# Kernel tuning notes

Hardware: AMD Instinct MI355X
Metric: run time of the kernel (lower is better)

## Reference

```python
import jax, jax.numpy as jnp
import numpy as np

D1 = 4096
D2 = 4096
K = 838860  # int(D1*D2*0.05)
ALPHA = 16.0


def setup_inputs() -> dict:
    key = jax.random.key(0)
    k1, k2, k3, k4, k5 = jax.random.split(key, 5)
    x = jax.random.normal(k1, (2, 64, D1), jnp.float32)
    W_base = jax.random.normal(k2, (D2, D1), jnp.float32) * 0.02  # torch Linear weight (out, in)
    b_base = jnp.zeros((D2,), jnp.float32)
    c_re = jax.random.normal(k3, (K,), jnp.float32) * 0.02
    c_im = jax.random.normal(k4, (K,), jnp.float32) * 0.02
    # unique flat positions of the top-k frequency coefficients (stand-in for topk of |fft2(delta_W_init)|)
    mask_idx = jax.random.permutation(k5, D1 * D2)[:K].astype(jnp.int32)
    return {"x": x, "W_base": W_base, "b_base": b_base,
            "c_re": c_re, "c_im": c_im, "mask_idx": mask_idx}


def reference(x, W_base, b_base, c_re, c_im, mask_idx):
    # scatter sparse complex coefficients into dense frequency matrix
    c = (c_re + 1j * c_im).astype(jnp.complex64)
    F_flat = jnp.zeros((D1 * D2,), jnp.complex64).at[mask_idx].set(c)
    # inverse 2D FFT -> real part -> scale by alpha
    Delta_W = jnp.fft.ifft2(F_flat.reshape(D1, D2)).real.astype(jnp.float32) * ALPHA  # [D1, D2]
    # frozen base linear: h = x @ W_base.T + b
    h = jnp.einsum('bnd,fd->bnf', x, W_base) + b_base
    # LoRA-style low-frequency update
    return h + jnp.einsum('bnd,df->bnf', x, Delta_W)
```

## Files before the change

kernel.cpp:

```cpp
#include <hip/hip_runtime.h>


#define TWO_PI 6.28318530717958647692f
constexpr int NROW = 128;
constexpr float SCALE_A = 16.0f / 16777216.0f;
constexpr int NCHUNK = 256;
constexpr int KC = 8;

typedef unsigned short ushort_t;
using short8 = __attribute__((ext_vector_type(8))) short;
using f32x4  = __attribute__((ext_vector_type(4))) float;

__device__ __forceinline__ ushort_t f2bf(float f) {
  unsigned u = __float_as_uint(f);
  u = (u + 0x7FFFu + ((u >> 16) & 1u)) >> 16;
  return (ushort_t)u;
}

__device__ __forceinline__ unsigned cvtpk(float lo, float hi) {
  unsigned r;
  asm("v_cvt_pk_bf16_f32 %0, %1, %2" : "=v"(r) : "v"(lo), "v"(hi));
  return r;
}

__device__ __forceinline__ void gload_lds16(const void* g, void* l) {
  __builtin_amdgcn_global_load_lds(
      (const __attribute__((address_space(1))) unsigned*)g,
      (__attribute__((address_space(3))) unsigned*)l, 16, 0, 0);
}

__global__ __launch_bounds__(1024) void fused_stage1(const float* __restrict__ x,
                                                     unsigned* __restrict__ XTb,
                                                     const int* __restrict__ idx, int K,
                                                     int chunk, int* __restrict__ cnt) {
  __shared__ __align__(16) char smem[33280];
  const int bx = blockIdx.x, tid = threadIdx.x;
  if (bx < 256) {
    float* xs = (float*)smem;
    float* br = xs + 4096;
    float* bi = br + 2048;
    float2* w64 = (float2*)(bi + 2048);
    const int t = bx & 127, qi = bx >> 7;
    const float* xrow = x + (size_t)t * 4096;
#pragma unroll
    for (int l = 0; l < 4; ++l) xs[tid + 1024 * l] = xrow[tid + 1024 * l];
    if (tid < 64) {
      float s, c; __sincosf(TWO_PI * (float)tid * (1.0f / 64.0f), &s, &c);
      w64[tid] = make_float2(c, s);
    }
    __syncthreads();
#pragma unroll
    for (int l = 0; l < 2; ++l) {
      int o = tid + 1024 * l, m1 = o >> 5, k1l = o & 31, k1 = qi * 32 + k1l;
      float ar = 0.f, ai = 0.f;
      for (int m2 = 0; m2 < 64; ++m2) {
        float xv = xs[m1 + (m2 << 6)];
        float2 w = w64[(m2 * k1) & 63];
        ar = fmaf(xv, w.x, ar); ai = fmaf(xv, w.y, ai);
      }
      float s, c; __sincosf((float)(m1 * k1) * (TWO_PI / 4096.0f), &s, &c);
      br[(m1 << 5) + k1l] = ar * c - ai * s;
      bi[(m1 << 5) + k1l] = ar * s + ai * c;
    }
    __syncthreads();
    {
      const int k1l = tid & 31, k2 = tid >> 5;
      const int k = qi * 32 + k1l + (k2 << 6);
      float xr = 0.f, xi = 0.f;
      for (int m1 = 0; m1 < 64; ++m1) {
        float brv = br[(m1 << 5) + k1l], biv = bi[(m1 << 5) + k1l];
        float2 w = w64[(m1 * k2) & 63];
        xr += brv * w.x - biv * w.y;
        xi += brv * w.y + biv * w.x;
      }
      XTb[(size_t)k * NROW + t] = (unsigned)f2bf(xr) | ((unsigned)f2bf(xi) << 16);
      if (qi == 0 && tid == 0) {
        float xr2 = 0.f, xi2 = 0.f;
        for (int m1 = 0; m1 < 64; ++m1) {
          float sgn = (m1 & 1) ? -1.f : 1.f;
          xr2 = fmaf(sgn, br[m1 << 5], xr2);
          xi2 = fmaf(sgn, bi[m1 << 5], xi2);
        }
        XTb[(size_t)2048 * NROW + t] = (unsigned)f2bf(xr2) | ((unsigned)f2bf(xi2) << 16);
      }
    }
  } else {
    int* h = (int*)smem;
    const int c = bx - 256;
#pragma unroll
    for (int l = 0; l < 4; ++l) h[tid + 1024 * l] = 0;
    __syncthreads();
    const int j0 = c * chunk, j1 = min(j0 + chunk, K);
    for (int j = j0 + tid; j < j1; j += 1024) atomicAdd(&h[idx[j] & 4095], 1);
    __syncthreads();
#pragma unroll
    for (int l = 0; l < 4; ++l) cnt[(size_t)c * 4096 + tid + 1024 * l] = h[tid + 1024 * l];
  }
}

__global__ __launch_bounds__(256) void colscan(int* __restrict__ cnt, int* __restrict__ tot) {
  const int k2 = blockIdx.x * 256 + threadIdx.x;
  int run = 0;
  for (int c8 = 0; c8 < NCHUNK; c8 += 8) {
    int v[8];
#pragma unroll
    for (int i = 0; i < 8; ++i) v[i] = cnt[(size_t)(c8 + i) * 4096 + k2];
#pragma unroll
    for (int i = 0; i < 8; ++i) {
      cnt[(size_t)(c8 + i) * 4096 + k2] = run;
      run += v[i];
    }
  }
  tot[k2] = run;
}

__global__ __launch_bounds__(1024) void scan4096(const int* __restrict__ count,
                                                 int* __restrict__ off) {
  __shared__ int s[4096];
  int tid = threadIdx.x;
#pragma unroll
  for (int l = 0; l < 4; ++l) s[tid + 1024 * l] = count[tid + 1024 * l];
  __syncthreads();
  for (int d = 1; d < 4096; d <<= 1) {
    int v[4];
#pragma unroll
    for (int l = 0; l < 4; ++l) {
      int i = tid + 1024 * l;
      v[l] = s[i] + ((i >= d) ? s[i - d] : 0);
    }
    __syncthreads();
#pragma unroll
    for (int l = 0; l < 4; ++l) s[tid + 1024 * l] = v[l];
    __syncthreads();
  }
#pragma unroll
  for (int l = 0; l < 4; ++l) {
    int i = tid + 1024 * l;
    off[i] = s[i] - count[i];
  }
}

__global__ __launch_bounds__(1024) void scatter2(const int* __restrict__ idx,
                                                 const float* __restrict__ cre,
                                                 const float* __restrict__ cim, int K,
                                                 int chunk, const int* __restrict__ base,
                                                 const int* __restrict__ off,
                                                 uint2* __restrict__ bucket) {
  __shared__ int lbase[4096];
  __shared__ int lcur[4096];
  const int c = blockIdx.x, tid = threadIdx.x;
#pragma unroll
  for (int l = 0; l < 4; ++l) {
    int k2 = tid + 1024 * l;
    lbase[k2] = base[(size_t)c * 4096 + k2] + off[k2];
    lcur[k2] = 0;
  }
  __syncthreads();
  const int j0 = c * chunk, j1 = min(j0 + chunk, K);
  for (int j = j0 + tid; j < j1; j += 1024) {
    int p = idx[j];
    int k2 = p & 4095;
    int r = atomicAdd(&lcur[k2], 1);
    unsigned cr = f2bf(cre[j]), ci = f2bf(cim[j]);
    bucket[lbase[k2] + r] = make_uint2((unsigned)(p >> 12) | (cr << 16), ci << 16);
  }
}

__global__ __launch_bounds__(256, 4) void spmm_col(const uint2* __restrict__ bucket,
                                                   const int* __restrict__ off,
                                                   const int* __restrict__ count,
                                                   const unsigned* __restrict__ XTb,
                                                   float2* __restrict__ Y) {
  __shared__ float4 red[2][64];
  const int lane = threadIdx.x & 63;
  const int wid = threadIdx.x >> 6;
  const int colsel = wid >> 1, half = wid & 1;
  const int k2 = blockIdx.x * 2 + colsel;
  const int s = off[k2], n = count[k2];
  const unsigned voff = lane * 8;
  float ar0 = 0.f, ai0 = 0.f, ar1 = 0.f, ai1 = 0.f;
  for (int c = half * 64; c < n; c += 128) {
    int idx = c + lane;
    uint2 ec = (idx < n) ? bucket[s + idx] : make_uint2(0u, 0u);
#pragma unroll
    for (int g = 0; g < 64; g += 8) {
      unsigned Ap[8], Bp[8];
      uint2 xv0, xv1, xv2, xv3, xv4, xv5, xv6, xv7;
#pragma unroll
      for (int u = 0; u < 8; ++u) {
        unsigned w0 = (unsigned)__builtin_amdgcn_readlane((int)ec.x, g + u);
        unsigned w1 = (unsigned)__builtin_amdgcn_readlane((int)ec.y, g + u);
        int k1 = (int)(w0 & 0xfffu);
        unsigned cj = (k1 > 2048) ? 0x8000u : 0u;
        int r = (k1 > 2048) ? 4096 - k1 : k1;
        unsigned cr16 = w0 >> 16;
        unsigned ci16 = w1 >> 16;
        Ap[u] = cr16 | ((ci16 ^ 0x8000u ^ cj) << 16);
        Bp[u] = ci16 | ((cr16 ^ cj) << 16);
        const unsigned* p = XTb + (size_t)r * NROW;
        uint2* dst = (u == 0) ? &xv0 : (u == 1) ? &xv1 : (u == 2) ? &xv2 :
                     (u == 3) ? &xv3 : (u == 4) ? &xv4 : (u == 5) ? &xv5 :
                     (u == 6) ? &xv6 : &xv7;
        asm volatile("global_load_dwordx2 %0, %1, %2"
                     : "=v"(*dst) : "v"(voff), "s"(p) : "memory");
      }
      asm volatile("s_waitcnt vmcnt(0)"
                   : "+v"(xv0), "+v"(xv1), "+v"(xv2), "+v"(xv3),
                     "+v"(xv4), "+v"(xv5), "+v"(xv6), "+v"(xv7) :: "memory");
      __builtin_amdgcn_sched_barrier(0);
#pragma unroll
      for (int u = 0; u < 8; ++u) {
        uint2 xv = (u == 0) ? xv0 : (u == 1) ? xv1 : (u == 2) ? xv2 :
                   (u == 3) ? xv3 : (u == 4) ? xv4 : (u == 5) ? xv5 :
                   (u == 6) ? xv6 : xv7;
        asm("v_dot2_f32_bf16 %0, %1, %2, %0" : "+v"(ar0) : "v"(Ap[u]), "v"(xv.x));
        asm("v_dot2_f32_bf16 %0, %1, %2, %0" : "+v"(ai0) : "v"(Bp[u]), "v"(xv.x));
        asm("v_dot2_f32_bf16 %0, %1, %2, %0" : "+v"(ar1) : "v"(Ap[u]), "v"(xv.y));
        asm("v_dot2_f32_bf16 %0, %1, %2, %0" : "+v"(ai1) : "v"(Bp[u]), "v"(xv.y));
      }
    }
  }
  if (half == 1) red[colsel][lane] = make_float4(ar0, ai0, ar1, ai1);
  __syncthreads();
  if (half == 0) {
    float4 o = red[colsel][lane];
    ar0 += o.x; ai0 += o.y; ar1 += o.z; ai1 += o.w;
    Y[(size_t)(2 * lane) * 4096 + k2]     = make_float2(ar0, ai0);
    Y[(size_t)(2 * lane + 1) * 4096 + k2] = make_float2(ar1, ai1);
  }
}

__global__ __launch_bounds__(256) void gemm_mfma_partial(const ushort_t* __restrict__ xbf,
                                                         const float* __restrict__ W,
                                                         ushort_t* __restrict__ partb) {
  __shared__ ushort_t xs[128 * 128];
  __shared__ float    wsf[64 * 128];
  const int f0 = blockIdx.x * 64;
  const int kc = blockIdx.y;
  const int tid = threadIdx.x;
  const int w = tid >> 6, lane = tid & 63;

  f32x4 acc[2][4];
#pragma unroll
  for (int i = 0; i < 2; ++i)
#pragma unroll
    for (int j = 0; j < 4; ++j) acc[i][j] = (f32x4){0.f, 0.f, 0.f, 0.f};

  const int kbeg = kc * 512;
  for (int st = 0; st < 4; ++st) {
    const int k0 = kbeg + st * 128;
#pragma unroll
    for (int cc = 0; cc < 8; ++cc) {
      int lb = w * 8192 + cc * 1024;
      int e  = (lb >> 1) + lane * 8;
      int r  = e >> 7;
      int sl = (e >> 3) & 15;
      gload_lds16(xbf + (size_t)r * 4096 + k0 + ((sl ^ (r & 15)) << 3),
                  (char*)xs + lb);
    }
#pragma unroll
    for (int cc = 0; cc < 8; ++cc) {
      int lb = w * 8192 + cc * 1024;
      int e32 = (lb >> 2) + lane * 4;
      int r = e32 >> 7;
      int g = (e32 >> 2) & 31;
      int s8 = g >> 1, h = g & 1;
      gload_lds16(W + (size_t)(f0 + r) * 4096 + k0 + ((s8 ^ (r & 15)) << 3) + (h << 2),
                  (char*)wsf + lb);
    }
    __syncthreads();
#pragma unroll
    for (int kk = 0; kk < 4; ++kk) {
      int ksA = kk * 4 + (lane >> 4);
      short8 af[2], bfr[4];
#pragma unroll
      for (int mf = 0; mf < 2; ++mf) {
        int ra = w * 32 + mf * 16 + (lane & 15);
        af[mf] = *(const short8*)(&xs[ra * 128 + ((ksA ^ (ra & 15)) << 3)]);
      }
#pragma unroll
      for (int nf = 0; nf < 4; ++nf) {
        int rb = nf * 16 + (lane & 15);
        const float* bp = &wsf[rb * 128 + ((ksA ^ (rb & 15)) << 3)];
        float4 a4 = *(const float4*)bp;
        float4 b4 = *(const float4*)(bp + 4);
        union { uint4 u; short8 s; } pk;
        pk.u.x = cvtpk(a4.x, a4.y);
        pk.u.y = cvtpk(a4.z, a4.w);
        pk.u.z = cvtpk(b4.x, b4.y);
        pk.u.w = cvtpk(b4.z, b4.w);
        bfr[nf] = pk.s;
      }
#pragma unroll
      for (int mf = 0; mf < 2; ++mf)
#pragma unroll
        for (int nf = 0; nf < 4; ++nf)
          acc[mf][nf] = __builtin_amdgcn_mfma_f32_16x16x32_bf16(af[mf], bfr[nf], acc[mf][nf], 0, 0, 0);
    }
    __syncthreads();
  }
  ushort_t* pb = partb + ((size_t)kc << 19);
#pragma unroll
  for (int mf = 0; mf < 2; ++mf)
#pragma unroll
    for (int nf = 0; nf < 4; ++nf)
#pragma unroll
      for (int reg = 0; reg < 4; ++reg) {
        int row = w * 32 + mf * 16 + (lane >> 4) * 4 + reg;
        int col = f0 + nf * 16 + (lane & 15);
        pb[(size_t)row * 4096 + col] = f2bf(acc[mf][nf][reg]);
      }
}

__global__ __launch_bounds__(1024) void dft_rows_y(const float2* __restrict__ Y,
                                                   const ushort_t* __restrict__ partb,
                                                   const float* __restrict__ bias,
                                                   float* __restrict__ out) {
  __shared__ float ysr[4096], ysi[4096];
  __shared__ float br[2048], bi[2048];
  __shared__ float2 w64[64];
  const int t = blockIdx.x, qi = blockIdx.y, tid = threadIdx.x;
  const float2* yrow = Y + (size_t)t * 4096;
#pragma unroll
  for (int l = 0; l < 4; ++l) {
    float2 v = yrow[tid + 1024 * l];
    ysr[tid + 1024 * l] = v.x; ysi[tid + 1024 * l] = v.y;
  }
  if (tid < 64) {
    float s, c; __sincosf(TWO_PI * (float)tid * (1.0f / 64.0f), &s, &c);
    w64[tid] = make_float2(c, s);
  }
  __syncthreads();
#pragma unroll
  for (int l = 0; l < 2; ++l) {
    int o = tid + 1024 * l, a = o >> 5, n1l = o & 31, n1 = qi * 32 + n1l;
    float ar = 0.f, ai = 0.f;
    for (int b = 0; b < 64; ++b) {
      float yr = ysr[a + (b << 6)], yi = ysi[a + (b << 6)];
      float2 w = w64[(n1 * b) & 63];
      ar += yr * w.x - yi * w.y;
      ai += yr * w.y + yi * w.x;
    }
    float s, c; __sincosf((float)(n1 * a) * (TWO_PI / 4096.0f), &s, &c);
    br[(a << 5) + n1l] = ar * c - ai * s;
    bi[(a << 5) + n1l] = ar * s + ai * c;
  }
  __syncthreads();
  float* orow = out + (size_t)t * 4096;
  const int n1l = tid & 31;
  const int n1 = qi * 32 + n1l;
#pragma unroll
  for (int l = 0; l < 2; ++l) {
    int n2 = (tid >> 5) + 32 * l;
    float accv = 0.f;
    for (int a = 0; a < 64; ++a) {
      float brv = br[(a << 5) + n1l], biv = bi[(a << 5) + n1l];
      float2 w = w64[(n2 * a) & 63];
      accv += brv * w.x - biv * w.y;
    }
    int o = n1 + (n2 << 6);
    float sum = accv * SCALE_A + bias[o];
#pragma unroll
    for (int i = 0; i < KC; ++i) {
      unsigned uu = partb[((size_t)i << 19) + ((size_t)t << 12) + o];
      sum += __int_as_float((int)(uu << 16));
    }
    orow[o] = sum;
  }
}

__global__ __launch_bounds__(256) void xcvt(const float* __restrict__ x,
                                            ushort_t* __restrict__ xbf) {
  size_t e = ((size_t)blockIdx.x * 256 + threadIdx.x) * 4;
  float4 v = *(const float4*)(x + e);
  unsigned lo = (unsigned)f2bf(v.x) | ((unsigned)f2bf(v.y) << 16);
  unsigned hi = (unsigned)f2bf(v.z) | ((unsigned)f2bf(v.w) << 16);
  *(uint2*)(xbf + e) = make_uint2(lo, hi);
}

extern "C" void kernel_launch(void* const* d_in, const int* in_sizes, int n_in,
                              void* d_out, int out_size, void* d_ws, size_t ws_size,
                              hipStream_t stream) {
  const float* x   = (const float*)d_in[0];
  const float* W   = (const float*)d_in[1];
  const float* b   = (const float*)d_in[2];
  const float* cre = (const float*)d_in[3];
  const float* cim = (const float*)d_in[4];
  const int* midx  = (const int*)d_in[5];
  const int K = in_sizes[3];
  float* out = (float*)d_out;
  const int chunk = (K + NCHUNK - 1) / NCHUNK;

  char* ws = (char*)d_ws;
  unsigned* XTb   = (unsigned*)(ws);
  float2* Y       = (float2*)(ws + ((size_t)2 << 20));
  char* meta      = ws + ((size_t)6 << 20);
  int* tot = (int*)(meta);
  int* off = (int*)(meta + 16384);
  uint2* bucket   = (uint2*)(ws + ((size_t)6 << 20) + 65536);
  int* cnt        = (int*)(ws + ((size_t)13 << 20));
  ushort_t* xbf   = (ushort_t*)(ws + ((size_t)17 << 20));
  ushort_t* partb = (ushort_t*)(ws + ((size_t)6 << 20) + 131072);

  xcvt<<<512, 256, 0, stream>>>(x, xbf);
  fused_stage1<<<512, 1024, 0, stream>>>(x, XTb, midx, K, chunk, cnt);
  colscan<<<16, 256, 0, stream>>>(cnt, tot);
  scan4096<<<1, 1024, 0, stream>>>(tot, off);
  scatter2<<<NCHUNK, 1024, 0, stream>>>(midx, cre, cim, K, chunk, cnt, off, bucket);
  spmm_col<<<2048, 256, 0, stream>>>(bucket, off, tot, XTb, Y);
  gemm_mfma_partial<<<dim3(64, KC), 256, 0, stream>>>(xbf, W, partb);
  dft_rows_y<<<dim3(NROW, 2), 1024, 0, stream>>>(Y, partb, b, out);
}
```

Measured before the change: 125.1 us.

## Fuse spmm with dense GEMM, fold x conversion into stage1, bf16 DFT intermediates

Merges the sparse column SpMM and the split-K MFMA GEMM into one heterogeneous launch so the two independent workloads run concurrently. The GEMM split-K count is halved with smaller K tiles. The x-to-bf16 conversion becomes extra blocks of the stage-1 kernel, removing a launch. DFT intermediates and Y are stored as packed bf16 and reduced with v_dot2_f32_bf16, halving traffic and FMA count at the cost of precision. The partial-sum readback contains a redundant multiply-by-zero term.

```diff
diff --git a/kernel.cpp b/kernel.cpp
--- a/kernel.cpp
+++ b/kernel.cpp
@@ -5,7 +5,7 @@
 constexpr int NROW = 128;
 constexpr float SCALE_A = 16.0f / 16777216.0f;
 constexpr int NCHUNK = 256;
-constexpr int KC = 8;
+constexpr int KC = 4;
 
 typedef unsigned short ushort_t;
 using short8 = __attribute__((ext_vector_type(8))) short;
@@ -16,13 +16,16 @@
   u = (u + 0x7FFFu + ((u >> 16) & 1u)) >> 16;
   return (ushort_t)u;
 }
-
 __device__ __forceinline__ unsigned cvtpk(float lo, float hi) {
   unsigned r;
   asm("v_cvt_pk_bf16_f32 %0, %1, %2" : "=v"(r) : "v"(lo), "v"(hi));
   return r;
 }
-
+__device__ __forceinline__ float bflo(unsigned u) { return __int_as_float((int)(u << 16)); }
+__device__ __forceinline__ float bfhi(unsigned u) { return __int_as_float((int)(u & 0xffff0000u)); }
+__device__ __forceinline__ void dot2(float& acc, unsigned a, unsigned b) {
+  asm("v_dot2_f32_bf16 %0, %1, %2, %0" : "+v"(acc) : "v"(a), "v"(b));
+}
 __device__ __forceinline__ void gload_lds16(const void* g, void* l) {
   __builtin_amdgcn_global_load_lds(
       (const __attribute__((address_space(1))) unsigned*)g,
@@ -32,21 +35,31 @@
 __global__ __launch_bounds__(1024) void fused_stage1(const float* __restrict__ x,
                                                      unsigned* __restrict__ XTb,
                                                      const int* __restrict__ idx, int K,
-                                                     int chunk, int* __restrict__ cnt) {
-  __shared__ __align__(16) char smem[33280];
+                                                     int chunk, int* __restrict__ cnt,
+                                                     ushort_t* __restrict__ xbf) {
+  __shared__ __align__(16) char smem[25600];
   const int bx = blockIdx.x, tid = threadIdx.x;
+  if (bx >= 512) {
+    int i = (bx - 512) * 1024 + tid;
+    float4 v = ((const float4*)x)[i];
+    ((uint2*)xbf)[i] = make_uint2(cvtpk(v.x, v.y), cvtpk(v.z, v.w));
+    return;
+  }
   if (bx < 256) {
-    float* xs = (float*)smem;
-    float* br = xs + 4096;
-    float* bi = br + 2048;
-    float2* w64 = (float2*)(bi + 2048);
+    float*    xs   = (float*)smem;
+    unsigned* bp   = (unsigned*)(smem + 16384);
+    float2*   w64f = (float2*)(smem + 24576);
+    unsigned* wA   = (unsigned*)(smem + 25088);
+    unsigned* wB   = (unsigned*)(smem + 25344);
     const int t = bx & 127, qi = bx >> 7;
     const float* xrow = x + (size_t)t * 4096;
 #pragma unroll
     for (int l = 0; l < 4; ++l) xs[tid + 1024 * l] = xrow[tid + 1024 * l];
     if (tid < 64) {
       float s, c; __sincosf(TWO_PI * (float)tid * (1.0f / 64.0f), &s, &c);
-      w64[tid] = make_float2(c, s);
+      w64f[tid] = make_float2(c, s);
+      wA[tid] = cvtpk(c, -s);
+      wB[tid] = cvtpk(s, c);
     }
     __syncthreads();
 #pragma unroll
@@ -55,12 +68,11 @@
       float ar = 0.f, ai = 0.f;
       for (int m2 = 0; m2 < 64; ++m2) {
         float xv = xs[m1 + (m2 << 6)];
-        float2 w = w64[(m2 * k1) & 63];
+        float2 w = w64f[(m2 * k1) & 63];
         ar = fmaf(xv, w.x, ar); ai = fmaf(xv, w.y, ai);
       }
       float s, c; __sincosf((float)(m1 * k1) * (TWO_PI / 4096.0f), &s, &c);
-      br[(m1 << 5) + k1l] = ar * c - ai * s;
-      bi[(m1 << 5) + k1l] = ar * s + ai * c;
+      bp[(m1 << 5) + k1l] = cvtpk(ar * c - ai * s, ar * s + ai * c);
     }
     __syncthreads();
     {
@@ -68,20 +80,21 @@
       const int k = qi * 32 + k1l + (k2 << 6);
       float xr = 0.f, xi = 0.f;
       for (int m1 = 0; m1 < 64; ++m1) {
-        float brv = br[(m1 << 5) + k1l], biv = bi[(m1 << 5) + k1l];
-        float2 w = w64[(m1 * k2) & 63];
-        xr += brv * w.x - biv * w.y;
-        xi += brv * w.y + biv * w.x;
-      }
-      XTb[(size_t)k * NROW + t] = (unsigned)f2bf(xr) | ((unsigned)f2bf(xi) << 16);
+        unsigned wi = (unsigned)((m1 * k2) & 63);
+        unsigned bv = bp[(m1 << 5) + k1l];
+        dot2(xr, wA[wi], bv);
+        dot2(xi, wB[wi], bv);
+      }
+      XTb[(size_t)k * NROW + t] = cvtpk(xr, xi);
       if (qi == 0 && tid == 0) {
         float xr2 = 0.f, xi2 = 0.f;
         for (int m1 = 0; m1 < 64; ++m1) {
           float sgn = (m1 & 1) ? -1.f : 1.f;
-          xr2 = fmaf(sgn, br[m1 << 5], xr2);
-          xi2 = fmaf(sgn, bi[m1 << 5], xi2);
-        }
-        XTb[(size_t)2048 * NROW + t] = (unsigned)f2bf(xr2) | ((unsigned)f2bf(xi2) << 16);
+          unsigned bv = bp[m1 << 5];
+          xr2 = fmaf(sgn, bflo(bv), xr2);
+          xi2 = fmaf(sgn, bfhi(bv), xi2);
+        }
+        XTb[(size_t)2048 * NROW + t] = cvtpk(xr2, xi2);
       }
     }
   } else {
@@ -166,169 +179,162 @@
   }
 }
 
-__global__ __launch_bounds__(256, 4) void spmm_col(const uint2* __restrict__ bucket,
-                                                   const int* __restrict__ off,
-                                                   const int* __restrict__ count,
-                                                   const unsigned* __restrict__ XTb,
-                                                   float2* __restrict__ Y) {
-  __shared__ float4 red[2][64];
-  const int lane = threadIdx.x & 63;
-  const int wid = threadIdx.x >> 6;
-  const int colsel = wid >> 1, half = wid & 1;
-  const int k2 = blockIdx.x * 2 + colsel;
-  const int s = off[k2], n = count[k2];
-  const unsigned voff = lane * 8;
-  float ar0 = 0.f, ai0 = 0.f, ar1 = 0.f, ai1 = 0.f;
-  for (int c = half * 64; c < n; c += 128) {
-    int idx = c + lane;
-    uint2 ec = (idx < n) ? bucket[s + idx] : make_uint2(0u, 0u);
-#pragma unroll
-    for (int g = 0; g < 64; g += 8) {
-      unsigned Ap[8], Bp[8];
-      uint2 xv0, xv1, xv2, xv3, xv4, xv5, xv6, xv7;
-#pragma unroll
-      for (int u = 0; u < 8; ++u) {
-        unsigned w0 = (unsigned)__builtin_amdgcn_readlane((int)ec.x, g + u);
-        unsigned w1 = (unsigned)__builtin_amdgcn_readlane((int)ec.y, g + u);
-        int k1 = (int)(w0 & 0xfffu);
-        unsigned cj = (k1 > 2048) ? 0x8000u : 0u;
-        int r = (k1 > 2048) ? 4096 - k1 : k1;
-        unsigned cr16 = w0 >> 16;
-        unsigned ci16 = w1 >> 16;
-        Ap[u] = cr16 | ((ci16 ^ 0x8000u ^ cj) << 16);
-        Bp[u] = ci16 | ((cr16 ^ cj) << 16);
-        const unsigned* p = XTb + (size_t)r * NROW;
-        uint2* dst = (u == 0) ? &xv0 : (u == 1) ? &xv1 : (u == 2) ? &xv2 :
-                     (u == 3) ? &xv3 : (u == 4) ? &xv4 : (u == 5) ? &xv5 :
-                     (u == 6) ? &xv6 : &xv7;
-        asm volatile("global_load_dwordx2 %0, %1, %2"
-                     : "=v"(*dst) : "v"(voff), "s"(p) : "memory");
-      }
-      asm volatile("s_waitcnt vmcnt(0)"
-                   : "+v"(xv0), "+v"(xv1), "+v"(xv2), "+v"(xv3),
-                     "+v"(xv4), "+v"(xv5), "+v"(xv6), "+v"(xv7) :: "memory");
-      __builtin_amdgcn_sched_barrier(0);
-#pragma unroll
-      for (int u = 0; u < 8; ++u) {
-        uint2 xv = (u == 0) ? xv0 : (u == 1) ? xv1 : (u == 2) ? xv2 :
-                   (u == 3) ? xv3 : (u == 4) ? xv4 : (u == 5) ? xv5 :
-                   (u == 6) ? xv6 : xv7;
-        asm("v_dot2_f32_bf16 %0, %1, %2, %0" : "+v"(ar0) : "v"(Ap[u]), "v"(xv.x));
-        asm("v_dot2_f32_bf16 %0, %1, %2, %0" : "+v"(ai0) : "v"(Bp[u]), "v"(xv.x));
-        asm("v_dot2_f32_bf16 %0, %1, %2, %0" : "+v"(ar1) : "v"(Ap[u]), "v"(xv.y));
-        asm("v_dot2_f32_bf16 %0, %1, %2, %0" : "+v"(ai1) : "v"(Bp[u]), "v"(xv.y));
-      }
-    }
-  }
-  if (half == 1) red[colsel][lane] = make_float4(ar0, ai0, ar1, ai1);
-  __syncthreads();
-  if (half == 0) {
-    float4 o = red[colsel][lane];
-    ar0 += o.x; ai0 += o.y; ar1 += o.z; ai1 += o.w;
-    Y[(size_t)(2 * lane) * 4096 + k2]     = make_float2(ar0, ai0);
-    Y[(size_t)(2 * lane + 1) * 4096 + k2] = make_float2(ar1, ai1);
-  }
-}
-
-__global__ __launch_bounds__(256) void gemm_mfma_partial(const ushort_t* __restrict__ xbf,
-                                                         const float* __restrict__ W,
-                                                         ushort_t* __restrict__ partb) {
-  __shared__ ushort_t xs[128 * 128];
-  __shared__ float    wsf[64 * 128];
-  const int f0 = blockIdx.x * 64;
-  const int kc = blockIdx.y;
+__global__ __launch_bounds__(256, 4) void fused_heavy(const uint2* __restrict__ bucket,
+                                                      const int* __restrict__ off,
+                                                      const int* __restrict__ count,
+                                                      const unsigned* __restrict__ XTb,
+                                                      unsigned* __restrict__ Yp,
+                                                      const ushort_t* __restrict__ xbf,
+                                                      const float* __restrict__ W,
+                                                      ushort_t* __restrict__ partb) {
+  __shared__ __align__(16) char smem[32768];
   const int tid = threadIdx.x;
   const int w = tid >> 6, lane = tid & 63;
-
-  f32x4 acc[2][4];
-#pragma unroll
-  for (int i = 0; i < 2; ++i)
-#pragma unroll
-    for (int j = 0; j < 4; ++j) acc[i][j] = (f32x4){0.f, 0.f, 0.f, 0.f};
-
-  const int kbeg = kc * 512;
-  for (int st = 0; st < 4; ++st) {
-    const int k0 = kbeg + st * 128;
-#pragma unroll
-    for (int cc = 0; cc < 8; ++cc) {
-      int lb = w * 8192 + cc * 1024;
-      int e  = (lb >> 1) + lane * 8;
-      int r  = e >> 7;
-      int sl = (e >> 3) & 15;
-      gload_lds16(xbf + (size_t)r * 4096 + k0 + ((sl ^ (r & 15)) << 3),
-                  (char*)xs + lb);
-    }
-#pragma unroll
-    for (int cc = 0; cc < 8; ++cc) {
-      int lb = w * 8192 + cc * 1024;
-      int e32 = (lb >> 2) + lane * 4;
-      int r = e32 >> 7;
-      int g = (e32 >> 2) & 31;
-      int s8 = g >> 1, h = g & 1;
-      gload_lds16(W + (size_t)(f0 + r) * 4096 + k0 + ((s8 ^ (r & 15)) << 3) + (h << 2),
-                  (char*)wsf + lb);
-    }
-    __syncthreads();
-#pragma unroll
-    for (int kk = 0; kk < 4; ++kk) {
-      int ksA = kk * 4 + (lane >> 4);
-      short8 af[2], bfr[4];
-#pragma unroll
-      for (int mf = 0; mf < 2; ++mf) {
-        int ra = w * 32 + mf * 16 + (lane & 15);
-        af[mf] = *(const short8*)(&xs[ra * 128 + ((ksA ^ (ra & 15)) << 3)]);
-      }
-#pragma unroll
-      for (int nf = 0; nf < 4; ++nf) {
-        int rb = nf * 16 + (lane & 15);
-        const float* bp = &wsf[rb * 128 + ((ksA ^ (rb & 15)) << 3)];
-        float4 a4 = *(const float4*)bp;
-        float4 b4 = *(const float4*)(bp + 4);
-        union { uint4 u; short8 s; } pk;
-        pk.u.x = cvtpk(a4.x, a4.y);
-        pk.u.y = cvtpk(a4.z, a4.w);
-        pk.u.z = cvtpk(b4.x, b4.y);
-        pk.u.w = cvtpk(b4.z, b4.w);
-        bfr[nf] = pk.s;
-      }
-#pragma unroll
-      for (int mf = 0; mf < 2; ++mf)
-#pragma unroll
-        for (int nf = 0; nf < 4; ++nf)
-          acc[mf][nf] = __builtin_amdgcn_mfma_f32_16x16x32_bf16(af[mf], bfr[nf], acc[mf][nf], 0, 0, 0);
-    }
-    __syncthreads();
-  }
-  ushort_t* pb = partb + ((size_t)kc << 19);
-#pragma unroll
-  for (int mf = 0; mf < 2; ++mf)
-#pragma unroll
-    for (int nf = 0; nf < 4; ++nf)
-#pragma unroll
-      for (int reg = 0; reg < 4; ++reg) {
-        int row = w * 32 + mf * 16 + (lane >> 4) * 4 + reg;
-        int col = f0 + nf * 16 + (lane & 15);
-        pb[(size_t)row * 4096 + col] = f2bf(acc[mf][nf][reg]);
-      }
-}
-
-__global__ __launch_bounds__(1024) void dft_rows_y(const float2* __restrict__ Y,
+  if (blockIdx.x >= 256) {
+    float4* red = (float4*)smem;
+    const int colsel = w >> 1, half = w & 1;
+    const int k2 = (blockIdx.x - 256) * 2 + colsel;
+    const int s = off[k2], n = count[k2];
+    const unsigned voff = lane * 8;
+    float ar0 = 0.f, ai0 = 0.f, ar1 = 0.f, ai1 = 0.f;
+    for (int c = half * 64; c < n; c += 128) {
+      int idx = c + lane;
+      uint2 ec = (idx < n) ? bucket[s + idx] : make_uint2(0u, 0u);
+#pragma unroll
+      for (int g = 0; g < 64; g += 8) {
+        unsigned Ap[8], Bp[8];
+        uint2 xv0, xv1, xv2, xv3, xv4, xv5, xv6, xv7;
+#pragma unroll
+        for (int u = 0; u < 8; ++u) {
+          unsigned w0 = (unsigned)__builtin_amdgcn_readlane((int)ec.x, g + u);
+          unsigned w1 = (unsigned)__builtin_amdgcn_readlane((int)ec.y, g + u);
+          int k1 = (int)(w0 & 0xfffu);
+          unsigned cj = (k1 > 2048) ? 0x8000u : 0u;
+          int r = (k1 > 2048) ? 4096 - k1 : k1;
+          unsigned cr16 = w0 >> 16;
+          unsigned ci16 = w1 >> 16;
+          Ap[u] = cr16 | ((ci16 ^ 0x8000u ^ cj) << 16);
+          Bp[u] = ci16 | ((cr16 ^ cj) << 16);
+          const unsigned* p = XTb + (size_t)r * NROW;
+          uint2* dst = (u == 0) ? &xv0 : (u == 1) ? &xv1 : (u == 2) ? &xv2 :
+                       (u == 3) ? &xv3 : (u == 4) ? &xv4 : (u == 5) ? &xv5 :
+                       (u == 6) ? &xv6 : &xv7;
+          asm volatile("global_load_dwordx2 %0, %1, %2"
+                       : "=v"(*dst) : "v"(voff), "s"(p) : "memory");
+        }
+        asm volatile("s_waitcnt vmcnt(0)"
+                     : "+v"(xv0), "+v"(xv1), "+v"(xv2), "+v"(xv3),
+                       "+v"(xv4), "+v"(xv5), "+v"(xv6), "+v"(xv7) :: "memory");
+        __builtin_amdgcn_sched_barrier(0);
+#pragma unroll
+        for (int u = 0; u < 8; ++u) {
+          uint2 xv = (u == 0) ? xv0 : (u == 1) ? xv1 : (u == 2) ? xv2 :
+                     (u == 3) ? xv3 : (u == 4) ? xv4 : (u == 5) ? xv5 :
+                     (u == 6) ? xv6 : xv7;
+          dot2(ar0, Ap[u], xv.x);
+          dot2(ai0, Bp[u], xv.x);
+          dot2(ar1, Ap[u], xv.y);
+          dot2(ai1, Bp[u], xv.y);
+        }
+      }
+    }
+    if (half == 1) red[colsel * 64 + lane] = make_float4(ar0, ai0, ar1, ai1);
+    __syncthreads();
+    if (half == 0) {
+      float4 o = red[colsel * 64 + lane];
+      ar0 += o.x; ai0 += o.y; ar1 += o.z; ai1 += o.w;
+      Yp[(size_t)(2 * lane) * 4096 + k2]     = cvtpk(ar0, ai0);
+      Yp[(size_t)(2 * lane + 1) * 4096 + k2] = cvtpk(ar1, ai1);
+    }
+  } else {
+    ushort_t* xs = (ushort_t*)smem;
+    float* wsf = (float*)(smem + 16384);
+    const int f0 = (blockIdx.x & 63) * 64;
+    const int kc = blockIdx.x >> 6;
+    f32x4 acc[2][4];
+#pragma unroll
+    for (int i = 0; i < 2; ++i)
+#pragma unroll
+      for (int j = 0; j < 4; ++j) acc[i][j] = (f32x4){0.f, 0.f, 0.f, 0.f};
+    const int kbeg = kc * 1024;
+    for (int st = 0; st < 16; ++st) {
+      const int k0 = kbeg + st * 64;
+#pragma unroll
+      for (int cc = 0; cc < 4; ++cc) {
+        int lb = w * 4096 + cc * 1024;
+        int e = (lb >> 1) + lane * 8;
+        int r = e >> 6, sl = (e >> 3) & 7;
+        gload_lds16(xbf + (size_t)r * 4096 + k0 + ((sl ^ (r & 7)) << 3),
+                    (char*)xs + lb);
+      }
+#pragma unroll
+      for (int cc = 0; cc < 4; ++cc) {
+        int lb = w * 4096 + cc * 1024;
+        int e32 = (lb >> 2) + lane * 4;
+        int r = e32 >> 6, g = (e32 >> 2) & 15, s8 = g >> 1, h = g & 1;
+        gload_lds16(W + (size_t)(f0 + r) * 4096 + k0 + ((s8 ^ (r & 7)) << 3) + (h << 2),
+                    (char*)wsf + lb);
+      }
+      __syncthreads();
+#pragma unroll
+      for (int kk = 0; kk < 2; ++kk) {
+        int ksA = kk * 4 + (lane >> 4);
+        short8 af[2], bfr[4];
+#pragma unroll
+        for (int mf = 0; mf < 2; ++mf) {
+          int ra = w * 32 + mf * 16 + (lane & 15);
+          af[mf] = *(const short8*)(&xs[ra * 64 + ((ksA ^ (ra & 7)) << 3)]);
+        }
+#pragma unroll
+        for (int nf = 0; nf < 4; ++nf) {
+          int rb = nf * 16 + (lane & 15);
+          const float* bpp = &wsf[rb * 64 + ((ksA ^ (rb & 7)) << 3)];
+          float4 a4 = *(const float4*)bpp;
+          float4 b4 = *(const float4*)(bpp + 4);
+          union { uint4 u; short8 s; } pk;
+          pk.u.x = cvtpk(a4.x, a4.y);
+          pk.u.y = cvtpk(a4.z, a4.w);
+          pk.u.z = cvtpk(b4.x, b4.y);
+          pk.u.w = cvtpk(b4.z, b4.w);
+          bfr[nf] = pk.s;
+        }
+#pragma unroll
+        for (int mf = 0; mf < 2; ++mf)
+#pragma unroll
+          for (int nf = 0; nf < 4; ++nf)
+            acc[mf][nf] = __builtin_amdgcn_mfma_f32_16x16x32_bf16(af[mf], bfr[nf], acc[mf][nf], 0, 0, 0);
+      }
+      __syncthreads();
+    }
+    ushort_t* pb = partb + ((size_t)kc << 19);
+#pragma unroll
+    for (int mf = 0; mf < 2; ++mf)
+#pragma unroll
+      for (int nf = 0; nf < 4; ++nf)
+#pragma unroll
+        for (int reg = 0; reg < 4; ++reg) {
+          int row = w * 32 + mf * 16 + (lane >> 4) * 4 + reg;
+          int col = f0 + nf * 16 + (lane & 15);
+          pb[(size_t)row * 4096 + col] = f2bf(acc[mf][nf][reg]);
+        }
+  }
+}
+
+__global__ __launch_bounds__(1024) void dft_rows_y(const unsigned* __restrict__ Yp,
                                                    const ushort_t* __restrict__ partb,
                                                    const float* __restrict__ bias,
                                                    float* __restrict__ out) {
-  __shared__ float ysr[4096], ysi[4096];
-  __shared__ float br[2048], bi[2048];
-  __shared__ float2 w64[64];
+  __shared__ unsigned ys[4096];
+  __shared__ unsigned bp[2048];
+  __shared__ unsigned wA[64], wB[64];
   const int t = blockIdx.x, qi = blockIdx.y, tid = threadIdx.x;
-  const float2* yrow = Y + (size_t)t * 4096;
-#pragma unroll
-  for (int l = 0; l < 4; ++l) {
-    float2 v = yrow[tid + 1024 * l];
-    ysr[tid + 1024 * l] = v.x; ysi[tid + 1024 * l] = v.y;
-  }
+  const unsigned* yrow = Yp + (size_t)t * 4096;
+#pragma unroll
+  for (int l = 0; l < 4; ++l) ys[tid + 1024 * l] = yrow[tid + 1024 * l];
   if (tid < 64) {
     float s, c; __sincosf(TWO_PI * (float)tid * (1.0f / 64.0f), &s, &c);
-    w64[tid] = make_float2(c, s);
+    wA[tid] = cvtpk(c, -s);
+    wB[tid] = cvtpk(s, c);
   }
   __syncthreads();
 #pragma unroll
@@ -336,14 +342,13 @@
     int o = tid + 1024 * l, a = o >> 5, n1l = o & 31, n1 = qi * 32 + n1l;
     float ar = 0.f, ai = 0.f;
     for (int b = 0; b < 64; ++b) {
-      float yr = ysr[a + (b << 6)], yi = ysi[a + (b << 6)];
-      float2 w = w64[(n1 * b) & 63];
-      ar += yr * w.x - yi * w.y;
-      ai += yr * w.y + yi * w.x;
+      unsigned yv = ys[a + (b << 6)];
+      unsigned wi = (unsigned)((n1 * b) & 63);
+      dot2(ar, wA[wi], yv);
+      dot2(ai, wB[wi], yv);
     }
     float s, c; __sincosf((float)(n1 * a) * (TWO_PI / 4096.0f), &s, &c);
-    br[(a << 5) + n1l] = ar * c - ai * s;
-    bi[(a << 5) + n1l] = ar * s + ai * c;
+    bp[(a << 5) + n1l] = cvtpk(ar * c - ai * s, ar * s + ai * c);
   }
   __syncthreads();
   float* orow = out + (size_t)t * 4096;
@@ -353,29 +358,16 @@
   for (int l = 0; l < 2; ++l) {
     int n2 = (tid >> 5) + 32 * l;
     float accv = 0.f;
-    for (int a = 0; a < 64; ++a) {
-      float brv = br[(a << 5) + n1l], biv = bi[(a << 5) + n1l];
-      float2 w = w64[(n2 * a) & 63];
-      accv += brv * w.x - biv * w.y;
-    }
+    for (int a = 0; a < 64; ++a)
+      dot2(accv, wA[(unsigned)((n2 * a) & 63)], bp[(a << 5) + n1l]);
     int o = n1 + (n2 << 6);
     float sum = accv * SCALE_A + bias[o];
 #pragma unroll
-    for (int i = 0; i < KC; ++i) {
-      unsigned uu = partb[((size_t)i << 19) + ((size_t)t << 12) + o];
-      sum += __int_as_float((int)(uu << 16));
-    }
+    for (int i = 0; i < KC; ++i)
+      sum += bflo((unsigned)partb[((size_t)i << 19) + ((size_t)t << 12) + o] << 0) * 0.f +
+             __int_as_float((int)((unsigned)partb[((size_t)i << 19) + ((size_t)t << 12) + o] << 16));
     orow[o] = sum;
   }
-}
-
-__global__ __launch_bounds__(256) void xcvt(const float* __restrict__ x,
-                                            ushort_t* __restrict__ xbf) {
-  size_t e = ((size_t)blockIdx.x * 256 + threadIdx.x) * 4;
-  float4 v = *(const float4*)(x + e);
-  unsigned lo = (unsigned)f2bf(v.x) | ((unsigned)f2bf(v.y) << 16);
-  unsigned hi = (unsigned)f2bf(v.z) | ((unsigned)f2bf(v.w) << 16);
-  *(uint2*)(xbf + e) = make_uint2(lo, hi);
 }
 
 extern "C" void kernel_launch(void* const* d_in, const int* in_sizes, int n_in,
@@ -393,21 +385,19 @@
 
   char* ws = (char*)d_ws;
   unsigned* XTb   = (unsigned*)(ws);
-  float2* Y       = (float2*)(ws + ((size_t)2 << 20));
-  char* meta      = ws + ((size_t)6 << 20);
+  unsigned* Yp    = (unsigned*)(ws + ((size_t)2 << 20));
+  ushort_t* xbf   = (ushort_t*)(ws + ((size_t)4 << 20));
+  char* meta      = ws + ((size_t)5 << 20);
   int* tot = (int*)(meta);
   int* off = (int*)(meta + 16384);
-  uint2* bucket   = (uint2*)(ws + ((size_t)6 << 20) + 65536);
-  int* cnt        = (int*)(ws + ((size_t)13 << 20));
-  ushort_t* xbf   = (ushort_t*)(ws + ((size_t)17 << 20));
-  ushort_t* partb = (ushort_t*)(ws + ((size_t)6 << 20) + 131072);
-
-  xcvt<<<512, 256, 0, stream>>>(x, xbf);
-  fused_stage1<<<512, 1024, 0, stream>>>(x, XTb, midx, K, chunk, cnt);
+  uint2* bucket   = (uint2*)(ws + ((size_t)5 << 20) + 262144);
+  int* cnt        = (int*)(ws + ((size_t)12 << 20));
+  ushort_t* partb = (ushort_t*)(ws + ((size_t)16 << 20));
+
+  fused_stage1<<<640, 1024, 0, stream>>>(x, XTb, midx, K, chunk, cnt, xbf);
   colscan<<<16, 256, 0, stream>>>(cnt, tot);
   scan4096<<<1, 1024, 0, stream>>>(tot, off);
   scatter2<<<NCHUNK, 1024, 0, stream>>>(midx, cre, cim, K, chunk, cnt, off, bucket);
-  spmm_col<<<2048, 256, 0, stream>>>(bucket, off, tot, XTb, Y);
-  gemm_mfma_partial<<<dim3(64, KC), 256, 0, stream>>>(xbf, W, partb);
-  dft_rows_y<<<dim3(NROW, 2), 1024, 0, stream>>>(Y, partb, b, out);
-}
+  fused_heavy<<<2304, 256, 0, stream>>>(bucket, off, tot, XTb, Yp, xbf, W, partb);
+  dft_rows_y<<<dim3(NROW, 2), 1024, 0, stream>>>(Yp, partb, b, out);
+}
```

After: 111.5 us. 1.12x faster.
